# Performance work log

Hardware: AMD Instinct MI355X
Metric: run time of the kernel (lower is better)

Reference implementation:

```python
import jax, jax.numpy as jnp
import numpy as np
from jax import lax

HID = 1024   # hidden_size
NH = 16      # num_heads
NKV = 4      # num_kv_heads (GQA)
HD = 64      # head_dim
SPLIT = 64   # fixed attention split size
KS = 3       # dynamic conv kernel size


def setup_inputs() -> dict:
    key = jax.random.key(0)
    ks = jax.random.split(key, 9)
    s = 0.02
    return {
        "hidden_states": jax.random.normal(ks[0], (2, 2048, HID), jnp.float32),
        "w_q": jax.random.normal(ks[1], (NH * HD, HID), jnp.float32) * s,
        "w_k": jax.random.normal(ks[2], (NKV * HD, HID), jnp.float32) * s,
        "w_v": jax.random.normal(ks[3], (NKV * HD, HID), jnp.float32) * s,
        "w_o": jax.random.normal(ks[4], (HID, NH * HD), jnp.float32) * s,
        "w_kgen": jax.random.normal(ks[5], (KS, HID), jnp.float32) * s,   # kernel_gen Linear weight
        "b_kgen": jnp.zeros((KS,), jnp.float32),
        "w_conv": jax.random.normal(ks[6], (HID, 1, KS), jnp.float32) * s,  # depthwise conv (O, I/g=1, K)
        "b_conv": jnp.zeros((HID,), jnp.float32),
    }


def _dynamic_conv(x, w_kgen, b_kgen, w_conv, b_conv):
    # x: (B, S, H). context-adaptive scalar gate per batch item (strict path:
    # per-item sigmoid(dyn_weights).mean() is a scalar -> vectorized identically).
    context = x.mean(axis=1)                                   # (B, H)
    dyn = context @ w_kgen.T + b_kgen                          # (B, KS)
    gate = jax.nn.sigmoid(dyn).mean(axis=1)                    # (B,)
    x_t = x.transpose(0, 2, 1)                                 # (B, H, S)
    y = lax.conv_general_dilated(
        x_t, w_conv, window_strides=(1,), padding=[(KS // 2, KS // 2)],
        feature_group_count=HID, dimension_numbers=("NCH", "OIH", "NCH"))
    y = (y + b_conv[None, :, None]) * gate[:, None, None]      # (B, H, S)
    return y.transpose(0, 2, 1)                                # (B, S, H)


def _fixed_split_attention(x, w_q, w_k, w_v, w_o):
    B, S, _ = x.shape
    q = (x @ w_q.T).reshape(B, S, NH, HD).transpose(0, 2, 1, 3)    # (B, NH, S, D)
    k = (x @ w_k.T).reshape(B, S, NKV, HD).transpose(0, 2, 1, 3)   # (B, NKV, S, D)
    v = (x @ w_v.T).reshape(B, S, NKV, HD).transpose(0, 2, 1, 3)
    n_rep = NH // NKV
    k = jnp.repeat(k, n_rep, axis=1)                               # GQA repeat
    v = jnp.repeat(v, n_rep, axis=1)
    C = S // SPLIT                                                 # number of KV chunks
    kc = k.reshape(B, NH, C, SPLIT, HD)
    vc = v.reshape(B, NH, C, SPLIT, HD)
    scale = HD ** -0.5
    # chunk-local softmax (NOT a global softmax) -- faithful to strict path
    scores = jnp.einsum("bhqd,bhckd->bhcqk", q, kc) * scale        # (B,NH,C,S,SPLIT)
    w = jax.nn.softmax(scores.astype(jnp.float32), axis=-1).astype(q.dtype)
    chunk_out = jnp.einsum("bhcqk,bhckd->bhcqd", w, vc)            # (B,NH,C,S,D)
    sum_w = w.sum(axis=-1, keepdims=True)                          # (B,NH,C,S,1) ~= 1
    combined = (chunk_out * sum_w).sum(axis=2)                     # (B,NH,S,D)
    total = sum_w.sum(axis=2)                                      # (B,NH,S,1)
    out = combined / (total + 1e-9)
    out = out.transpose(0, 2, 1, 3).reshape(B, S, NH * HD)
    return out @ w_o.T


def reference(hidden_states, w_q, w_k, w_v, w_o, w_kgen, b_kgen, w_conv, b_conv):
    h = _dynamic_conv(hidden_states, w_kgen, b_kgen, w_conv, b_conv)
    return _fixed_split_attention(h, w_q, w_k, w_v, w_o)
```

## Files before the change

kernel.cpp:

```cpp
#include <hip/hip_runtime.h>

#define S_LEN 2048
#define HIDN 1024
#define NCHUNK 32

typedef __attribute__((ext_vector_type(8))) short bf16x8;
typedef __attribute__((ext_vector_type(4))) float f32x4;

__device__ __forceinline__ unsigned short f2bf(float f) {
  unsigned u = __float_as_uint(f);
  u += 0x7FFF + ((u >> 16) & 1);
  return (unsigned short)(u >> 16);
}

__device__ __forceinline__ int swz(int row, int col) {
  int u = ((col >> 3) ^ row ^ (row >> 3)) & 7;
  return row * 64 + (u << 3) + (col & 7);
}

__device__ __forceinline__ void gload_lds16(const void* g, void* l) {
  __builtin_amdgcn_global_load_lds(
      (const __attribute__((address_space(1))) unsigned int*)g,
      (__attribute__((address_space(3))) unsigned int*)l, 16, 0, 0);
}

__global__ __launch_bounds__(256) void ctx_partial_kernel(const float* __restrict__ x,
                                                          float* __restrict__ ctx) {
  int b = blockIdx.y, sc = blockIdx.x, t = threadIdx.x;
  float a0 = 0, a1 = 0, a2 = 0, a3 = 0;
  const float* base = x + ((size_t)b * S_LEN + sc * 32) * HIDN;
  for (int s = 0; s < 32; ++s) {
    const float* r = base + (size_t)s * HIDN;
    a0 += r[t]; a1 += r[t + 256]; a2 += r[t + 512]; a3 += r[t + 768];
  }
  atomicAdd(&ctx[b * HIDN + t], a0);
  atomicAdd(&ctx[b * HIDN + t + 256], a1);
  atomicAdd(&ctx[b * HIDN + t + 512], a2);
  atomicAdd(&ctx[b * HIDN + t + 768], a3);
}

__global__ __launch_bounds__(256) void gate_kernel(const float* __restrict__ ctx,
                                                   const float* __restrict__ w_kgen,
                                                   const float* __restrict__ b_kgen,
                                                   float* __restrict__ gate) {
  int b = blockIdx.x, t = threadIdx.x;
  __shared__ float red[256];
  float p[3] = {0.f, 0.f, 0.f};
  for (int c = t; c < 1024; c += 256) {
    float cv = ctx[b * HIDN + c] * (1.0f / 2048.0f);
    p[0] += cv * w_kgen[c];
    p[1] += cv * w_kgen[1024 + c];
    p[2] += cv * w_kgen[2048 + c];
  }
  float g = 0.f;
  for (int j = 0; j < 3; ++j) {
    red[t] = p[j];
    __syncthreads();
    for (int s = 128; s > 0; s >>= 1) {
      if (t < s) red[t] += red[t + s];
      __syncthreads();
    }
    if (t == 0) g += 1.0f / (1.0f + expf(-(red[0] + b_kgen[j])));
    __syncthreads();
  }
  if (t == 0) gate[b] = g * (1.0f / 3.0f);
}

__global__ __launch_bounds__(256) void conv_kernel(const float* __restrict__ x,
                                                   const float* __restrict__ w_conv,
                                                   const float* __restrict__ b_conv,
                                                   const float* __restrict__ gate,
                                                   unsigned short* __restrict__ hbuf) {
  int e = (blockIdx.x * 256 + threadIdx.x) * 4;
  int row = e >> 10, h0 = e & 1023;
  int s = row & (S_LEN - 1), b = row >> 11;
  const float* xr = x + (size_t)row * HIDN + h0;
  float xc[4], xm[4] = {0, 0, 0, 0}, xp[4] = {0, 0, 0, 0};
  *(float4*)xc = *(const float4*)xr;
  if (s > 0) *(float4*)xm = *(const float4*)(xr - HIDN);
  if (s < S_LEN - 1) *(float4*)xp = *(const float4*)(xr + HIDN);
  float g = gate[b];
  ushort4 o;
  unsigned short ov[4];
#pragma unroll
  for (int j = 0; j < 4; ++j) {
    int hh = h0 + j;
    float v = xm[j] * w_conv[hh * 3] + xc[j] * w_conv[hh * 3 + 1] +
              xp[j] * w_conv[hh * 3 + 2] + b_conv[hh];
    ov[j] = f2bf(v * g);
  }
  o.x = ov[0]; o.y = ov[1]; o.z = ov[2]; o.w = ov[3];
  *(ushort4*)(hbuf + e) = o;
}

__global__ __launch_bounds__(256) void wcast_kernel(const float* __restrict__ wq,
                                                    const float* __restrict__ wk,
                                                    const float* __restrict__ wv,
                                                    const float* __restrict__ wo,
                                                    unsigned short* __restrict__ W) {
  int e = (blockIdx.x * 256 + threadIdx.x) * 4;
  int row = e >> 10, col = e & 1023;
  const float* src;
  if (row < 1024) src = wq + (size_t)row * 1024 + col;
  else if (row < 1280) src = wk + (size_t)(row - 1024) * 1024 + col;
  else if (row < 1536) src = wv + (size_t)(row - 1280) * 1024 + col;
  else src = wo + (size_t)(row - 1536) * 1024 + col;
  float v[4];
  *(float4*)v = *(const float4*)src;
  ushort4 o;
  o.x = f2bf(v[0]); o.y = f2bf(v[1]); o.z = f2bf(v[2]); o.w = f2bf(v[3]);
  *(ushort4*)(W + e) = o;
}

template <typename OUT>
__global__ __launch_bounds__(256) void gemm_bt(const unsigned short* __restrict__ A,
                                               const unsigned short* __restrict__ Bw,
                                               OUT* __restrict__ C, int ldc) {
  __shared__ __align__(16) unsigned short As[128 * 32];
  __shared__ __align__(16) unsigned short Bs[128 * 32];
  const int t = threadIdx.x, w = t >> 6, l = t & 63;
  const int wr = w >> 1, wc = w & 1;
  const int tM = blockIdx.y * 128, tN = blockIdx.x * 128;
  const int lr = l >> 2, lc = (l & 3) * 8;
  f32x4 acc[4][4] = {};
  for (int k0 = 0; k0 < 1024; k0 += 32) {
#pragma unroll
    for (int i = 0; i < 2; ++i) {
      int seg = i * 4 + w;
      gload_lds16(A + (size_t)(tM + seg * 16 + lr) * 1024 + k0 + lc, &As[seg * 512]);
      gload_lds16(Bw + (size_t)(tN + seg * 16 + lr) * 1024 + k0 + lc, &Bs[seg * 512]);
    }
    __syncthreads();
    bf16x8 a[4], b[4];
#pragma unroll
    for (int m = 0; m < 4; ++m)
      a[m] = *(const bf16x8*)&As[(wr * 64 + m * 16 + (l & 15)) * 32 + (l >> 4) * 8];
#pragma unroll
    for (int n = 0; n < 4; ++n)
      b[n] = *(const bf16x8*)&Bs[(wc * 64 + n * 16 + (l & 15)) * 32 + (l >> 4) * 8];
#pragma unroll
    for (int m = 0; m < 4; ++m)
#pragma unroll
      for (int n = 0; n < 4; ++n)
        acc[m][n] = __builtin_amdgcn_mfma_f32_16x16x32_bf16(a[m], b[n], acc[m][n], 0, 0, 0);
    __syncthreads();
  }
#pragma unroll
  for (int m = 0; m < 4; ++m)
#pragma unroll
    for (int n = 0; n < 4; ++n)
#pragma unroll
      for (int r = 0; r < 4; ++r) {
        int row = tM + wr * 64 + m * 16 + (l >> 4) * 4 + r;
        int col = tN + wc * 64 + n * 16 + (l & 15);
        float v = acc[m][n][r];
        if constexpr (sizeof(OUT) == 2)
          C[(size_t)row * ldc + col] = (OUT)f2bf(v);
        else
          C[(size_t)row * ldc + col] = v;
      }
}

__global__ __launch_bounds__(256) void attn_kernel(const unsigned short* __restrict__ qkv,
                                                   unsigned short* __restrict__ attn) {
  const int qt = blockIdx.x, head = blockIdx.y, b = blockIdx.z;
  const int t = threadIdx.x, w = t >> 6, l = t & 63;
  const int hi = l >> 4, lo = l & 15;
  const int kv = head >> 2;
  __shared__ __align__(16) unsigned short Qs[4096], Ks[4096], Vt[4096];
  __shared__ __align__(16) unsigned short Ps[4096];

  const int sr = t >> 2, sc = (t & 3) * 16;
  {
    const unsigned short* src = qkv + (size_t)(b * S_LEN + qt * 64 + sr) * 1536 + head * 64 + sc;
    *(uint4*)&Qs[swz(sr, sc)] = *(const uint4*)src;
    *(uint4*)&Qs[swz(sr, sc + 8)] = *(const uint4*)(src + 8);
  }
  __syncthreads();
  bf16x8 qa[2];
#pragma unroll
  for (int kk = 0; kk < 2; ++kk)
    qa[kk] = *(const bf16x8*)&Qs[swz(w * 16 + lo, kk * 32 + hi * 8)];

  f32x4 oacc[4] = {};
  for (int c = 0; c < NCHUNK; ++c) {
    const size_t krow = (size_t)(b * S_LEN + c * 64 + sr) * 1536;
    const unsigned short* ksrc = qkv + krow + 1024 + kv * 64 + sc;
    *(uint4*)&Ks[swz(sr, sc)] = *(const uint4*)ksrc;
    *(uint4*)&Ks[swz(sr, sc + 8)] = *(const uint4*)(ksrc + 8);
    const unsigned short* vsrc = qkv + krow + 1280 + kv * 64 + sc;
    uint4 vraw[2];
    vraw[0] = *(const uint4*)vsrc;
    vraw[1] = *(const uint4*)(vsrc + 8);
    const unsigned short* vv = (const unsigned short*)vraw;
#pragma unroll
    for (int j = 0; j < 16; ++j) Vt[swz(sc + j, sr)] = vv[j];
    __syncthreads();

    f32x4 sacc[4] = {};
#pragma unroll
    for (int kk = 0; kk < 2; ++kk) {
#pragma unroll
      for (int f = 0; f < 4; ++f) {
        bf16x8 kb = *(const bf16x8*)&Ks[swz(f * 16 + lo, kk * 32 + hi * 8)];
        sacc[f] = __builtin_amdgcn_mfma_f32_16x16x32_bf16(qa[kk], kb, sacc[f], 0, 0, 0);
      }
    }

#pragma unroll
    for (int r = 0; r < 4; ++r) {
      float p[4], s = 0.f;
#pragma unroll
      for (int f = 0; f < 4; ++f) {
        p[f] = __expf(sacc[f][r] * 0.125f);
        s += p[f];
      }
#pragma unroll
      for (int off = 1; off < 16; off <<= 1) s += __shfl_xor(s, off);
      float inv = 1.0f / s;
#pragma unroll
      for (int f = 0; f < 4; ++f)
        Ps[w * 1024 + swz(hi * 4 + r, f * 16 + lo)] = f2bf(p[f] * inv);
    }

#pragma unroll
    for (int kk = 0; kk < 2; ++kk) {
      bf16x8 pa = *(const bf16x8*)&Ps[w * 1024 + swz(lo, kk * 32 + hi * 8)];
#pragma unroll
      for (int f = 0; f < 4; ++f) {
        bf16x8 vb = *(const bf16x8*)&Vt[swz(f * 16 + lo, kk * 32 + hi * 8)];
        oacc[f] = __builtin_amdgcn_mfma_f32_16x16x32_bf16(pa, vb, oacc[f], 0, 0, 0);
      }
    }
    __syncthreads();
  }

  const float invC = 1.0f / (32.0f + 1e-9f);
#pragma unroll
  for (int f = 0; f < 4; ++f)
#pragma unroll
    for (int r = 0; r < 4; ++r) {
      int row = b * S_LEN + qt * 64 + w * 16 + hi * 4 + r;
      int col = head * 64 + f * 16 + lo;
      attn[(size_t)row * HIDN + col] = f2bf(oacc[f][r] * invC);
    }
}

extern "C" void kernel_launch(void* const* d_in, const int* in_sizes, int n_in,
                              void* d_out, int out_size, void* d_ws, size_t ws_size,
                              hipStream_t stream) {
  const float* x = (const float*)d_in[0];
  const float* w_q = (const float*)d_in[1];
  const float* w_k = (const float*)d_in[2];
  const float* w_v = (const float*)d_in[3];
  const float* w_o = (const float*)d_in[4];
  const float* w_kgen = (const float*)d_in[5];
  const float* b_kgen = (const float*)d_in[6];
  const float* w_conv = (const float*)d_in[7];
  const float* b_conv = (const float*)d_in[8];
  float* out = (float*)d_out;

  char* ws = (char*)d_ws;
  float* ctx = (float*)ws;
  float* gate = (float*)(ws + 8192);
  unsigned short* W = (unsigned short*)(ws + 65536);
  unsigned short* h = (unsigned short*)(ws + 6291456);
  unsigned short* qkv = (unsigned short*)(ws + 14680064);
  unsigned short* attn = h;

  hipMemsetAsync(ctx, 0, 8192, stream);
  ctx_partial_kernel<<<dim3(64, 2), 256, 0, stream>>>(x, ctx);
  gate_kernel<<<2, 256, 0, stream>>>(ctx, w_kgen, b_kgen, gate);
  conv_kernel<<<4096, 256, 0, stream>>>(x, w_conv, b_conv, gate, h);
  wcast_kernel<<<2560, 256, 0, stream>>>(w_q, w_k, w_v, w_o, W);
  gemm_bt<unsigned short><<<dim3(12, 32), 256, 0, stream>>>(h, W, qkv, 1536);
  attn_kernel<<<dim3(32, 16, 2), 256, 0, stream>>>(qkv, attn);
  gemm_bt<float><<<dim3(8, 32), 256, 0, stream>>>(attn, W + 1536 * 1024, out, 1024);
}
```

Before: 258.9 us.

## Write transposed V from QKV GEMM and double-buffer attention K/V via async LDS loads

The QKV GEMM epilogue now writes V directly in transposed (head, dim, seq) layout and pre-scales Q by scale*log2(e). This lets the attention kernel use exp2 and drop the per-element LDS transpose of V. The attention kernel loads Q straight into registers and double-buffers K/V chunks in LDS with global_load_lds, prefetching the next chunk while computing the current one. It also swaps the MFMA operand order so the row sum needs only two shuffles, and writes P with packed bf16x2 stores. In exchange it uses more LDS and extra workspace for the transposed V, plus a strided scatter in the GEMM epilogue.

```diff
diff --git a/kernel.cpp b/kernel.cpp
--- a/kernel.cpp
+++ b/kernel.cpp
@@ -1,8 +1,10 @@
 #include <hip/hip_runtime.h>
+#include <hip/hip_bf16.h>
 
 #define S_LEN 2048
 #define HIDN 1024
 #define NCHUNK 32
+#define QKN 1280
 
 typedef __attribute__((ext_vector_type(8))) short bf16x8;
 typedef __attribute__((ext_vector_type(4))) float f32x4;
@@ -112,10 +114,12 @@
   *(ushort4*)(W + e) = o;
 }
 
-template <typename OUT>
+template <int MODE>
 __global__ __launch_bounds__(256) void gemm_bt(const unsigned short* __restrict__ A,
                                                const unsigned short* __restrict__ Bw,
-                                               OUT* __restrict__ C, int ldc) {
+                                               void* __restrict__ Cv,
+                                               unsigned short* __restrict__ vt,
+                                               int ldc) {
   __shared__ __align__(16) unsigned short As[128 * 32];
   __shared__ __align__(16) unsigned short Bs[128 * 32];
   const int t = threadIdx.x, w = t >> 6, l = t & 63;
@@ -145,97 +149,147 @@
         acc[m][n] = __builtin_amdgcn_mfma_f32_16x16x32_bf16(a[m], b[n], acc[m][n], 0, 0, 0);
     __syncthreads();
   }
-#pragma unroll
-  for (int m = 0; m < 4; ++m)
-#pragma unroll
-    for (int n = 0; n < 4; ++n)
-#pragma unroll
-      for (int r = 0; r < 4; ++r) {
-        int row = tM + wr * 64 + m * 16 + (l >> 4) * 4 + r;
-        int col = tN + wc * 64 + n * 16 + (l & 15);
-        float v = acc[m][n][r];
-        if constexpr (sizeof(OUT) == 2)
-          C[(size_t)row * ldc + col] = (OUT)f2bf(v);
-        else
-          C[(size_t)row * ldc + col] = v;
-      }
-}
-
-__global__ __launch_bounds__(256) void attn_kernel(const unsigned short* __restrict__ qkv,
-                                                   unsigned short* __restrict__ attn) {
+  if constexpr (MODE == 1) {
+    if (tN >= 1280) {
+#pragma unroll
+      for (int m = 0; m < 4; ++m)
+#pragma unroll
+        for (int n = 0; n < 4; ++n) {
+          int d = (tN - 1280) + wc * 64 + n * 16 + (l & 15);
+          int kvh = d >> 6, dl = d & 63;
+          int srow = tM + wr * 64 + m * 16 + (l >> 4) * 4;
+          int bb = srow >> 11, s = srow & (S_LEN - 1);
+          ushort4 o;
+          o.x = f2bf(acc[m][n][0]); o.y = f2bf(acc[m][n][1]);
+          o.z = f2bf(acc[m][n][2]); o.w = f2bf(acc[m][n][3]);
+          *(ushort4*)&vt[((size_t)((bb * 4 + kvh) * 64 + dl) << 11) + s] = o;
+        }
+    } else {
+      unsigned short* C = (unsigned short*)Cv;
+      const float sc = (tN < 1024) ? 0.18033688011112042f : 1.0f;
+#pragma unroll
+      for (int m = 0; m < 4; ++m)
+#pragma unroll
+        for (int n = 0; n < 4; ++n)
+#pragma unroll
+          for (int r = 0; r < 4; ++r) {
+            int row = tM + wr * 64 + m * 16 + (l >> 4) * 4 + r;
+            int col = tN + wc * 64 + n * 16 + (l & 15);
+            C[(size_t)row * ldc + col] = f2bf(acc[m][n][r] * sc);
+          }
+    }
+  } else {
+    float* C = (float*)Cv;
+#pragma unroll
+    for (int m = 0; m < 4; ++m)
+#pragma unroll
+      for (int n = 0; n < 4; ++n)
+#pragma unroll
+        for (int r = 0; r < 4; ++r) {
+          int row = tM + wr * 64 + m * 16 + (l >> 4) * 4 + r;
+          int col = tN + wc * 64 + n * 16 + (l & 15);
+          C[(size_t)row * ldc + col] = acc[m][n][r];
+        }
+  }
+}
+
+#define STAGE(cc, bb)                                                      \
+  do {                                                                     \
+    gload_lds16(kg0 + (size_t)(cc) * (64 * QKN), &ks[bb][w * 512]);        \
+    gload_lds16(kg1 + (size_t)(cc) * (64 * QKN), &ks[bb][2048 + w * 512]); \
+    gload_lds16(vg0 + (cc) * 64, &vs[bb][w * 512]);                        \
+    gload_lds16(vg1 + (cc) * 64, &vs[bb][2048 + w * 512]);                 \
+  } while (0)
+
+__global__ __launch_bounds__(256, 4) void attn_kernel(const unsigned short* __restrict__ qkv,
+                                                      const unsigned short* __restrict__ vt,
+                                                      unsigned short* __restrict__ attn) {
   const int qt = blockIdx.x, head = blockIdx.y, b = blockIdx.z;
   const int t = threadIdx.x, w = t >> 6, l = t & 63;
   const int hi = l >> 4, lo = l & 15;
   const int kv = head >> 2;
-  __shared__ __align__(16) unsigned short Qs[4096], Ks[4096], Vt[4096];
-  __shared__ __align__(16) unsigned short Ps[4096];
-
-  const int sr = t >> 2, sc = (t & 3) * 16;
-  {
-    const unsigned short* src = qkv + (size_t)(b * S_LEN + qt * 64 + sr) * 1536 + head * 64 + sc;
-    *(uint4*)&Qs[swz(sr, sc)] = *(const uint4*)src;
-    *(uint4*)&Qs[swz(sr, sc + 8)] = *(const uint4*)(src + 8);
-  }
+  __shared__ __align__(16) unsigned short ks[2][4096];
+  __shared__ __align__(16) unsigned short vs[2][4096];
+  __shared__ __align__(16) unsigned int psd[2048];
+
+  const unsigned short* qp =
+      qkv + (size_t)(b * S_LEN + qt * 64 + w * 16 + lo) * QKN + head * 64;
+  bf16x8 qa[2];
+  qa[0] = *(const bf16x8*)(qp + hi * 8);
+  qa[1] = *(const bf16x8*)(qp + 32 + hi * 8);
+
+  const int r0 = t >> 3, u0 = t & 7, r1 = r0 + 32;
+  const int x0 = (r0 ^ (r0 >> 3)) & 7, x1 = (r1 ^ (r1 >> 3)) & 7;
+  const unsigned short* kg0 =
+      qkv + (size_t)(b * S_LEN + r0) * QKN + 1024 + kv * 64 + ((u0 ^ x0) << 3);
+  const unsigned short* kg1 =
+      qkv + (size_t)(b * S_LEN + r1) * QKN + 1024 + kv * 64 + ((u0 ^ x1) << 3);
+  const unsigned short* vg0 =
+      vt + (size_t)((b * 4 + kv) * 64 + r0) * S_LEN + ((u0 ^ x0) << 3);
+  const unsigned short* vg1 =
+      vt + (size_t)((b * 4 + kv) * 64 + r1) * S_LEN + ((u0 ^ x1) << 3);
+
+  int pre[4][2];
+#pragma unroll
+  for (int f = 0; f < 4; ++f) {
+    int row = f * 16 + lo, rx = (row ^ (row >> 3)) & 7;
+#pragma unroll
+    for (int kk = 0; kk < 2; ++kk) pre[f][kk] = row * 64 + (((kk * 4 + hi) ^ rx) << 3);
+  }
+  const int key = (lo >> 1) << 2;
+  const int Xw = w * 512 + ((lo * 32 + hi * 2) ^ key);
+  const int Rb0 = w * 512 + lo * 32 + ((hi * 4) ^ key);
+  const int Rb1 = w * 512 + lo * 32 + ((16 + hi * 4) ^ key);
+
+  STAGE(0, 0);
   __syncthreads();
-  bf16x8 qa[2];
-#pragma unroll
-  for (int kk = 0; kk < 2; ++kk)
-    qa[kk] = *(const bf16x8*)&Qs[swz(w * 16 + lo, kk * 32 + hi * 8)];
 
   f32x4 oacc[4] = {};
+  int buf = 0;
   for (int c = 0; c < NCHUNK; ++c) {
-    const size_t krow = (size_t)(b * S_LEN + c * 64 + sr) * 1536;
-    const unsigned short* ksrc = qkv + krow + 1024 + kv * 64 + sc;
-    *(uint4*)&Ks[swz(sr, sc)] = *(const uint4*)ksrc;
-    *(uint4*)&Ks[swz(sr, sc + 8)] = *(const uint4*)(ksrc + 8);
-    const unsigned short* vsrc = qkv + krow + 1280 + kv * 64 + sc;
-    uint4 vraw[2];
-    vraw[0] = *(const uint4*)vsrc;
-    vraw[1] = *(const uint4*)(vsrc + 8);
-    const unsigned short* vv = (const unsigned short*)vraw;
-#pragma unroll
-    for (int j = 0; j < 16; ++j) Vt[swz(sc + j, sr)] = vv[j];
-    __syncthreads();
-
+    if (c + 1 < NCHUNK) STAGE(c + 1, buf ^ 1);
+    const unsigned short* kb = ks[buf];
+    const unsigned short* vb = vs[buf];
     f32x4 sacc[4] = {};
 #pragma unroll
-    for (int kk = 0; kk < 2; ++kk) {
-#pragma unroll
-      for (int f = 0; f < 4; ++f) {
-        bf16x8 kb = *(const bf16x8*)&Ks[swz(f * 16 + lo, kk * 32 + hi * 8)];
-        sacc[f] = __builtin_amdgcn_mfma_f32_16x16x32_bf16(qa[kk], kb, sacc[f], 0, 0, 0);
+    for (int kk = 0; kk < 2; ++kk)
+#pragma unroll
+      for (int f = 0; f < 4; ++f)
+        sacc[f] = __builtin_amdgcn_mfma_f32_16x16x32_bf16(
+            *(const bf16x8*)&kb[pre[f][kk]], qa[kk], sacc[f], 0, 0, 0);
+    float pv[4][4], ssum = 0.f;
+#pragma unroll
+    for (int f = 0; f < 4; ++f)
+#pragma unroll
+      for (int r = 0; r < 4; ++r) {
+        pv[f][r] = __builtin_amdgcn_exp2f(sacc[f][r]);
+        ssum += pv[f][r];
       }
-    }
-
-#pragma unroll
-    for (int r = 0; r < 4; ++r) {
-      float p[4], s = 0.f;
-#pragma unroll
-      for (int f = 0; f < 4; ++f) {
-        p[f] = __expf(sacc[f][r] * 0.125f);
-        s += p[f];
+    ssum += __shfl_xor(ssum, 16);
+    ssum += __shfl_xor(ssum, 32);
+    const float inv = __builtin_amdgcn_rcpf(ssum);
+#pragma unroll
+    for (int f = 0; f < 4; ++f)
+#pragma unroll
+      for (int rr = 0; rr < 2; ++rr) {
+        __hip_bfloat162 h2 = __float22bfloat162_rn(
+            make_float2(pv[f][2 * rr] * inv, pv[f][2 * rr + 1] * inv));
+        psd[Xw ^ (f * 8 + rr)] = *(unsigned*)&h2;
       }
-#pragma unroll
-      for (int off = 1; off < 16; off <<= 1) s += __shfl_xor(s, off);
-      float inv = 1.0f / s;
-#pragma unroll
-      for (int f = 0; f < 4; ++f)
-        Ps[w * 1024 + swz(hi * 4 + r, f * 16 + lo)] = f2bf(p[f] * inv);
-    }
-
-#pragma unroll
-    for (int kk = 0; kk < 2; ++kk) {
-      bf16x8 pa = *(const bf16x8*)&Ps[w * 1024 + swz(lo, kk * 32 + hi * 8)];
-#pragma unroll
-      for (int f = 0; f < 4; ++f) {
-        bf16x8 vb = *(const bf16x8*)&Vt[swz(f * 16 + lo, kk * 32 + hi * 8)];
-        oacc[f] = __builtin_amdgcn_mfma_f32_16x16x32_bf16(pa, vb, oacc[f], 0, 0, 0);
-      }
-    }
-    __syncthreads();
-  }
-
-  const float invC = 1.0f / (32.0f + 1e-9f);
+    bf16x8 pa0 = *(const bf16x8*)&psd[Rb0];
+    bf16x8 pa1 = *(const bf16x8*)&psd[Rb1];
+#pragma unroll
+    for (int f = 0; f < 4; ++f) {
+      oacc[f] = __builtin_amdgcn_mfma_f32_16x16x32_bf16(
+          pa0, *(const bf16x8*)&vb[pre[f][0]], oacc[f], 0, 0, 0);
+      oacc[f] = __builtin_amdgcn_mfma_f32_16x16x32_bf16(
+          pa1, *(const bf16x8*)&vb[pre[f][1]], oacc[f], 0, 0, 0);
+    }
+    __syncthreads();
+    buf ^= 1;
+  }
+
+  const float invC = 1.0f / 32.0f;
 #pragma unroll
   for (int f = 0; f < 4; ++f)
 #pragma unroll
@@ -245,6 +299,7 @@
       attn[(size_t)row * HIDN + col] = f2bf(oacc[f][r] * invC);
     }
 }
+#undef STAGE
 
 extern "C" void kernel_launch(void* const* d_in, const int* in_sizes, int n_in,
                               void* d_out, int out_size, void* d_ws, size_t ws_size,
@@ -266,14 +321,15 @@
   unsigned short* W = (unsigned short*)(ws + 65536);
   unsigned short* h = (unsigned short*)(ws + 6291456);
   unsigned short* qkv = (unsigned short*)(ws + 14680064);
-  unsigned short* attn = h;
+  unsigned short* vt = (unsigned short*)(ws + 25165824);
+  unsigned short* attnb = h;
 
   hipMemsetAsync(ctx, 0, 8192, stream);
   ctx_partial_kernel<<<dim3(64, 2), 256, 0, stream>>>(x, ctx);
   gate_kernel<<<2, 256, 0, stream>>>(ctx, w_kgen, b_kgen, gate);
   conv_kernel<<<4096, 256, 0, stream>>>(x, w_conv, b_conv, gate, h);
   wcast_kernel<<<2560, 256, 0, stream>>>(w_q, w_k, w_v, w_o, W);
-  gemm_bt<unsigned short><<<dim3(12, 32), 256, 0, stream>>>(h, W, qkv, 1536);
-  attn_kernel<<<dim3(32, 16, 2), 256, 0, stream>>>(qkv, attn);
-  gemm_bt<float><<<dim3(8, 32), 256, 0, stream>>>(attn, W + 1536 * 1024, out, 1024);
-}
+  gemm_bt<1><<<dim3(12, 32), 256, 0, stream>>>(h, W, qkv, vt, QKN);
+  attn_kernel<<<dim3(32, 16, 2), 256, 0, stream>>>(qkv, vt, attnb);
+  gemm_bt<0><<<dim3(8, 32), 256, 0, stream>>>(attnb, W + 1536 * 1024, out, nullptr, HIDN);
+}
```

New measurement: 218.2 us. 1.19x faster.
